# Performance work log

Measured on AMD Instinct MI355X. Metric: run time of the kernel, lower is better.

The kernel has to match this reference:

```python
import jax, jax.numpy as jnp
import numpy as np


def setup_inputs() -> dict:
    key = jax.random.key(0)
    ks = jax.random.split(key, 5)
    B, T, D = 1, 4096, 1024
    scale = 0.02
    return {
        "x": jax.random.normal(ks[0], (B, T, D), dtype=jnp.float32),
        "Wq": jax.random.normal(ks[1], (D, D), dtype=jnp.float32) * scale,
        "Wk": jax.random.normal(ks[2], (D, D), dtype=jnp.float32) * scale,
        "Wv": jax.random.normal(ks[3], (D, D), dtype=jnp.float32) * scale,
        "Wo": jax.random.normal(ks[4], (D, D), dtype=jnp.float32) * scale,
        "window": 128,
    }


def reference(x, Wq, Wk, Wv, Wo, window):
    # x: [B, T, D]; weights: [D, D] (torch nn.Linear layout: out = x @ W.T)
    B, T, D = x.shape
    H = 16
    dh = D // H

    def split_heads(y):
        # [B, T, D] -> [B, H, T, dh]
        return y.reshape(B, T, H, dh).transpose(0, 2, 1, 3)

    q = split_heads(x @ Wq.T)
    k = split_heads(x @ Wk.T)
    v = split_heads(x @ Wv.T)

    # causal sliding-window additive mask, [T, T]
    idx = jnp.arange(T)
    diff = idx[:, None] - idx[None, :]
    allowed = (diff >= 0) & (diff <= window)

    scale = 1.0 / jnp.sqrt(jnp.asarray(dh, dtype=q.dtype))
    scores = jnp.einsum('bhtd,bhsd->bhts', q, k) * scale  # [B,H,T,T]
    scores = jnp.where(allowed[None, None], scores, jnp.asarray(-jnp.inf, dtype=scores.dtype))
    attn = jax.nn.softmax(scores, axis=-1)
    out = jnp.einsum('bhts,bhsd->bhtd', attn, v)  # [B,H,T,dh]
    out = out.transpose(0, 2, 1, 3).reshape(B, T, D)
    return out @ Wo.T
```

## Files before the change

### kernel.cpp

```cpp
#include <hip/hip_runtime.h>
#include <hip/hip_bf16.h>

typedef __bf16 bf16_t;
typedef __bf16 bf16x8 __attribute__((ext_vector_type(8)));
typedef float f32x4 __attribute__((ext_vector_type(4)));

#define T_SEQ 4096
#define DM    1024
#define NH    16
#define DH    64

#define BM 128
#define BN 128
#define BK 64

typedef __attribute__((address_space(1))) void gvoid_t;
typedef __attribute__((address_space(3))) void lvoid_t;

__device__ __forceinline__ void gload_lds16(const void* g, void* l) {
    __builtin_amdgcn_global_load_lds((gvoid_t*)g, (lvoid_t*)l, 16, 0, 0);
}

__global__ __launch_bounds__(256) void cvt_all(
    const float* __restrict__ x,  const float* __restrict__ wq,
    const float* __restrict__ wk, const float* __restrict__ wv,
    const float* __restrict__ wo,
    bf16_t* __restrict__ xb, bf16_t* __restrict__ wqb, bf16_t* __restrict__ wkb,
    bf16_t* __restrict__ wvb, bf16_t* __restrict__ wob)
{
    const float* s; bf16_t* d; int n8;
    switch (blockIdx.y) {
        case 0:  s = x;  d = xb;  n8 = (T_SEQ * DM) / 8; break;
        case 1:  s = wq; d = wqb; n8 = (DM * DM) / 8;    break;
        case 2:  s = wk; d = wkb; n8 = (DM * DM) / 8;    break;
        case 3:  s = wv; d = wvb; n8 = (DM * DM) / 8;    break;
        default: s = wo; d = wob; n8 = (DM * DM) / 8;    break;
    }
    for (int i = blockIdx.x * 256 + threadIdx.x; i < n8; i += gridDim.x * 256) {
        float4 a = ((const float4*)s)[i * 2];
        float4 b = ((const float4*)s)[i * 2 + 1];
        bf16x8 o;
        o[0] = (bf16_t)a.x; o[1] = (bf16_t)a.y; o[2] = (bf16_t)a.z; o[3] = (bf16_t)a.w;
        o[4] = (bf16_t)b.x; o[5] = (bf16_t)b.y; o[6] = (bf16_t)b.z; o[7] = (bf16_t)b.w;
        ((bf16x8*)d)[i] = o;
    }
}

template<typename OT>
__global__ __launch_bounds__(256) void gemm_bt(
    const bf16_t* __restrict__ A,
    const bf16_t* __restrict__ B0, const bf16_t* __restrict__ B1, const bf16_t* __restrict__ B2,
    OT* __restrict__ C0, OT* __restrict__ C1, OT* __restrict__ C2,
    int M, int N, int K)
{
    const bf16_t* Bp; OT* Cp;
    if      (blockIdx.z == 0) { Bp = B0; Cp = C0; }
    else if (blockIdx.z == 1) { Bp = B1; Cp = C1; }
    else                      { Bp = B2; Cp = C2; }

    __shared__ __align__(16) bf16_t sA[BM * BK];
    __shared__ __align__(16) bf16_t sB[BN * BK];

    const int tid  = threadIdx.x;
    const int lane = tid & 63;
    const int w    = tid >> 6;
    const int wr   = w >> 1, wc = w & 1;
    const int l15  = lane & 15, lhi = lane >> 4;

    const int brow = blockIdx.x * BM;
    const int bcol = blockIdx.y * BN;

    f32x4 acc[4][4] = {};

    const int nkt = K / BK;
    for (int kt = 0; kt < nkt; ++kt) {
        __syncthreads();
        #pragma unroll
        for (int i = 0; i < 4; ++i) {
            int chunk = i * 256 + tid;
            int row   = chunk >> 3;
            int c8    = chunk & 7;
            int c8s   = c8 ^ (row & 7);
            const bf16_t* gA = A  + (size_t)(brow + row) * K + kt * BK + c8s * 8;
            const bf16_t* gB = Bp + (size_t)(bcol + row) * K + kt * BK + c8s * 8;
            gload_lds16(gA, &sA[chunk * 8]);
            gload_lds16(gB, &sB[chunk * 8]);
        }
        __syncthreads();

        #pragma unroll
        for (int kk = 0; kk < 2; ++kk) {
            bf16x8 af[4], bfr[4];
            #pragma unroll
            for (int m = 0; m < 4; ++m) {
                int r  = wr * 64 + m * 16 + l15;
                int c8 = (kk * 4 + lhi) ^ (r & 7);
                af[m] = *(const bf16x8*)(&sA[r * BK + c8 * 8]);
            }
            #pragma unroll
            for (int n = 0; n < 4; ++n) {
                int r  = wc * 64 + n * 16 + l15;
                int c8 = (kk * 4 + lhi) ^ (r & 7);
                bfr[n] = *(const bf16x8*)(&sB[r * BK + c8 * 8]);
            }
            #pragma unroll
            for (int m = 0; m < 4; ++m)
                #pragma unroll
                for (int n = 0; n < 4; ++n)
                    acc[m][n] = __builtin_amdgcn_mfma_f32_16x16x32_bf16(
                        af[m], bfr[n], acc[m][n], 0, 0, 0);
        }
    }

    #pragma unroll
    for (int m = 0; m < 4; ++m) {
        int rb = brow + wr * 64 + m * 16 + lhi * 4;
        #pragma unroll
        for (int n = 0; n < 4; ++n) {
            int cc = bcol + wc * 64 + n * 16 + l15;
            #pragma unroll
            for (int i = 0; i < 4; ++i)
                Cp[(size_t)(rb + i) * N + cc] = (OT)acc[m][n][i];
        }
    }
}

__global__ __launch_bounds__(256) void swa_attn(
    const bf16_t* __restrict__ Q, const bf16_t* __restrict__ K,
    const bf16_t* __restrict__ V, bf16_t* __restrict__ O,
    const int* __restrict__ winp)
{
    const int w    = winp[0];
    const int tid  = threadIdx.x;
    const int lane = tid & 63;
    const int wv   = tid >> 6;
    const int l15  = lane & 15, lhi = lane >> 4;
    const int h    = blockIdx.y;
    const int q0   = blockIdx.x * 64 + wv * 16;

    __shared__ __align__(16) bf16_t Pl[4][16 * 48];
    bf16_t* Pw = &Pl[wv][0];

    bf16x8 qf[2];
    #pragma unroll
    for (int c = 0; c < 2; ++c)
        qf[c] = *(const bf16x8*)(Q + (size_t)(q0 + l15) * DM + h * DH + c * 32 + lhi * 8);

    f32x4 acc[4] = {};
    f32x4 mrow = { -1e30f, -1e30f, -1e30f, -1e30f };
    f32x4 lrow = {};

    int ks = q0 - w; if (ks < 0) ks = 0; ks &= ~31;
    for (int kvs = ks; kvs <= q0 + 15; kvs += 32) {
        f32x4 s[2];
        #pragma unroll
        for (int hc = 0; hc < 2; ++hc) {
            f32x4 z = {};
            #pragma unroll
            for (int c = 0; c < 2; ++c) {
                bf16x8 kf = *(const bf16x8*)(K + (size_t)(kvs + hc * 16 + l15) * DM
                                               + h * DH + c * 32 + lhi * 8);
                z = __builtin_amdgcn_mfma_f32_16x16x32_bf16(qf[c], kf, z, 0, 0, 0);
            }
            #pragma unroll
            for (int i = 0; i < 4; ++i) {
                int qt = q0 + lhi * 4 + i;
                int kt = kvs + hc * 16 + l15;
                bool ok = (kt <= qt) && (qt - kt <= w);
                s[hc][i] = ok ? z[i] * 0.125f : -1e30f;
            }
        }
        f32x4 pm;
        #pragma unroll
        for (int i = 0; i < 4; ++i) pm[i] = fmaxf(s[0][i], s[1][i]);
        #pragma unroll
        for (int off = 1; off <= 8; off <<= 1)
            #pragma unroll
            for (int i = 0; i < 4; ++i)
                pm[i] = fmaxf(pm[i], __shfl_xor(pm[i], off));

        f32x4 mnew, alpha, p0, p1, rs;
        #pragma unroll
        for (int i = 0; i < 4; ++i) {
            mnew[i]  = fmaxf(mrow[i], pm[i]);
            alpha[i] = __expf(mrow[i] - mnew[i]);
            p0[i]    = __expf(s[0][i] - mnew[i]);
            p1[i]    = __expf(s[1][i] - mnew[i]);
            rs[i]    = p0[i] + p1[i];
        }
        #pragma unroll
        for (int off = 1; off <= 8; off <<= 1)
            #pragma unroll
            for (int i = 0; i < 4; ++i)
                rs[i] += __shfl_xor(rs[i], off);
        #pragma unroll
        for (int i = 0; i < 4; ++i) {
            lrow[i] = lrow[i] * alpha[i] + rs[i];
            mrow[i] = mnew[i];
        }
        #pragma unroll
        for (int nc = 0; nc < 4; ++nc)
            #pragma unroll
            for (int i = 0; i < 4; ++i) acc[nc][i] *= alpha[i];

        #pragma unroll
        for (int i = 0; i < 4; ++i) {
            int r = lhi * 4 + i;
            Pw[r * 48 + l15]      = (bf16_t)p0[i];
            Pw[r * 48 + 16 + l15] = (bf16_t)p1[i];
        }
        bf16x8 pa = *(const bf16x8*)(&Pw[l15 * 48 + lhi * 8]);

        #pragma unroll
        for (int nc = 0; nc < 4; ++nc) {
            bf16x8 vf;
            #pragma unroll
            for (int j = 0; j < 8; ++j)
                vf[j] = V[(size_t)(kvs + lhi * 8 + j) * DM + h * DH + nc * 16 + l15];
            acc[nc] = __builtin_amdgcn_mfma_f32_16x16x32_bf16(pa, vf, acc[nc], 0, 0, 0);
        }
    }

    #pragma unroll
    for (int nc = 0; nc < 4; ++nc)
        #pragma unroll
        for (int i = 0; i < 4; ++i) {
            float o = acc[nc][i] / lrow[i];
            O[(size_t)(q0 + lhi * 4 + i) * DM + h * DH + nc * 16 + l15] = (bf16_t)o;
        }
}

extern "C" void kernel_launch(void* const* d_in, const int* in_sizes, int n_in,
                              void* d_out, int out_size, void* d_ws, size_t ws_size,
                              hipStream_t stream)
{
    const float* x  = (const float*)d_in[0];
    const float* Wq = (const float*)d_in[1];
    const float* Wk = (const float*)d_in[2];
    const float* Wv = (const float*)d_in[3];
    const float* Wo = (const float*)d_in[4];
    const int*   wn = (const int*)d_in[5];
    float* out = (float*)d_out;

    bf16_t* ws = (bf16_t*)d_ws;
    const size_t nx = (size_t)T_SEQ * DM;
    const size_t nw = (size_t)DM * DM;
    bf16_t* xb  = ws;
    bf16_t* Wqb = xb + nx;
    bf16_t* Wkb = Wqb + nw;
    bf16_t* Wvb = Wkb + nw;
    bf16_t* Wob = Wvb + nw;
    bf16_t* Qb  = Wob + nw;
    bf16_t* Kb  = Qb + nx;
    bf16_t* Vb  = Kb + nx;
    bf16_t* Ab  = Vb + nx;

    dim3 g0(1024, 5, 1);
    cvt_all<<<g0, 256, 0, stream>>>(x, Wq, Wk, Wv, Wo, xb, Wqb, Wkb, Wvb, Wob);

    dim3 g1(T_SEQ / BM, DM / BN, 3);
    gemm_bt<bf16_t><<<g1, 256, 0, stream>>>(xb, Wqb, Wkb, Wvb, Qb, Kb, Vb, T_SEQ, DM, DM);

    dim3 g2(T_SEQ / 64, NH, 1);
    swa_attn<<<g2, 256, 0, stream>>>(Qb, Kb, Vb, Ab, wn);

    dim3 g3(T_SEQ / BM, DM / BN, 1);
    gemm_bt<float><<<g3, 256, 0, stream>>>(Ab, Wob, Wob, Wob, out, out, out, T_SEQ, DM, DM);
}
```

Before: 88.70 us.

## Process 32 query rows per wave and reuse K/V fragments across row groups

Each attention wave now handles two 16-row query groups over 64-key tiles. Every K and V fragment it loads feeds MFMAs for both groups, roughly halving global K/V traffic per query. The P staging buffer is enlarged and padded to hold the larger tile. The cost is higher register pressure, fewer blocks in the grid, and more masked work at the window edges. The conversion kernel's grid is also halved, which assumes it uses a grid-stride loop.

```diff
diff --git a/kernel.cpp b/kernel.cpp
--- a/kernel.cpp
+++ b/kernel.cpp
@@ -125,6 +125,7 @@
     }
 }
 
+#define PPAD 72
 __global__ __launch_bounds__(256) void swa_attn(
     const bf16_t* __restrict__ Q, const bf16_t* __restrict__ K,
     const bf16_t* __restrict__ V, bf16_t* __restrict__ O,
@@ -136,98 +137,139 @@
     const int wv   = tid >> 6;
     const int l15  = lane & 15, lhi = lane >> 4;
     const int h    = blockIdx.y;
-    const int q0   = blockIdx.x * 64 + wv * 16;
-
-    __shared__ __align__(16) bf16_t Pl[4][16 * 48];
+    const int q0   = blockIdx.x * 128 + wv * 32;
+
+    __shared__ __align__(16) bf16_t Pl[4][32 * PPAD];
     bf16_t* Pw = &Pl[wv][0];
 
-    bf16x8 qf[2];
+    const bf16_t* Qh = Q + (size_t)h * DH;
+    const bf16_t* Kh = K + (size_t)h * DH;
+    const bf16_t* Vh = V + (size_t)h * DH;
+
+    bf16x8 qf[2][2];
     #pragma unroll
-    for (int c = 0; c < 2; ++c)
-        qf[c] = *(const bf16x8*)(Q + (size_t)(q0 + l15) * DM + h * DH + c * 32 + lhi * 8);
-
-    f32x4 acc[4] = {};
-    f32x4 mrow = { -1e30f, -1e30f, -1e30f, -1e30f };
-    f32x4 lrow = {};
-
-    int ks = q0 - w; if (ks < 0) ks = 0; ks &= ~31;
-    for (int kvs = ks; kvs <= q0 + 15; kvs += 32) {
-        f32x4 s[2];
-        #pragma unroll
-        for (int hc = 0; hc < 2; ++hc) {
-            f32x4 z = {};
-            #pragma unroll
-            for (int c = 0; c < 2; ++c) {
-                bf16x8 kf = *(const bf16x8*)(K + (size_t)(kvs + hc * 16 + l15) * DM
-                                               + h * DH + c * 32 + lhi * 8);
-                z = __builtin_amdgcn_mfma_f32_16x16x32_bf16(qf[c], kf, z, 0, 0, 0);
-            }
+    for (int g = 0; g < 2; ++g)
+        #pragma unroll
+        for (int c = 0; c < 2; ++c)
+            qf[g][c] = *(const bf16x8*)(Qh + (size_t)(q0 + g * 16 + l15) * DM
+                                           + c * 32 + lhi * 8);
+
+    f32x4 acc[2][4] = {};
+    f32x4 mrow[2], lrow[2];
+    #pragma unroll
+    for (int g = 0; g < 2; ++g) {
+        mrow[g] = { -1e30f, -1e30f, -1e30f, -1e30f };
+        lrow[g] = {};
+    }
+
+    int ks = q0 - w; if (ks < 0) ks = 0; ks &= ~63;
+    for (int kvs = ks; kvs <= q0 + 31; kvs += 64) {
+        f32x4 s[2][4];
+        #pragma unroll
+        for (int hc = 0; hc < 4; ++hc) {
+            bf16x8 kf[2];
+            #pragma unroll
+            for (int c = 0; c < 2; ++c)
+                kf[c] = *(const bf16x8*)(Kh + (size_t)(kvs + hc * 16 + l15) * DM
+                                            + c * 32 + lhi * 8);
+            #pragma unroll
+            for (int g = 0; g < 2; ++g) {
+                f32x4 z = {};
+                z = __builtin_amdgcn_mfma_f32_16x16x32_bf16(qf[g][0], kf[0], z, 0, 0, 0);
+                z = __builtin_amdgcn_mfma_f32_16x16x32_bf16(qf[g][1], kf[1], z, 0, 0, 0);
+                #pragma unroll
+                for (int i = 0; i < 4; ++i) {
+                    int qt = q0 + g * 16 + lhi * 4 + i;
+                    int kt = kvs + hc * 16 + l15;
+                    bool ok = (kt <= qt) && (qt - kt <= w);
+                    s[g][hc][i] = ok ? z[i] * 0.125f : -1e30f;
+                }
+            }
+        }
+        #pragma unroll
+        for (int g = 0; g < 2; ++g) {
+            f32x4 pm;
+            #pragma unroll
+            for (int i = 0; i < 4; ++i)
+                pm[i] = fmaxf(fmaxf(s[g][0][i], s[g][1][i]),
+                              fmaxf(s[g][2][i], s[g][3][i]));
+            #pragma unroll
+            for (int off = 1; off <= 8; off <<= 1)
+                #pragma unroll
+                for (int i = 0; i < 4; ++i)
+                    pm[i] = fmaxf(pm[i], __shfl_xor(pm[i], off));
+
+            f32x4 mnew, alpha, rs;
             #pragma unroll
             for (int i = 0; i < 4; ++i) {
-                int qt = q0 + lhi * 4 + i;
-                int kt = kvs + hc * 16 + l15;
-                bool ok = (kt <= qt) && (qt - kt <= w);
-                s[hc][i] = ok ? z[i] * 0.125f : -1e30f;
-            }
-        }
-        f32x4 pm;
-        #pragma unroll
-        for (int i = 0; i < 4; ++i) pm[i] = fmaxf(s[0][i], s[1][i]);
-        #pragma unroll
-        for (int off = 1; off <= 8; off <<= 1)
-            #pragma unroll
-            for (int i = 0; i < 4; ++i)
-                pm[i] = fmaxf(pm[i], __shfl_xor(pm[i], off));
-
-        f32x4 mnew, alpha, p0, p1, rs;
-        #pragma unroll
-        for (int i = 0; i < 4; ++i) {
-            mnew[i]  = fmaxf(mrow[i], pm[i]);
-            alpha[i] = __expf(mrow[i] - mnew[i]);
-            p0[i]    = __expf(s[0][i] - mnew[i]);
-            p1[i]    = __expf(s[1][i] - mnew[i]);
-            rs[i]    = p0[i] + p1[i];
-        }
-        #pragma unroll
-        for (int off = 1; off <= 8; off <<= 1)
-            #pragma unroll
-            for (int i = 0; i < 4; ++i)
-                rs[i] += __shfl_xor(rs[i], off);
-        #pragma unroll
-        for (int i = 0; i < 4; ++i) {
-            lrow[i] = lrow[i] * alpha[i] + rs[i];
-            mrow[i] = mnew[i];
-        }
+                mnew[i]  = fmaxf(mrow[g][i], pm[i]);
+                alpha[i] = __expf(mrow[g][i] - mnew[i]);
+                rs[i]    = 0.f;
+            }
+            #pragma unroll
+            for (int hc = 0; hc < 4; ++hc)
+                #pragma unroll
+                for (int i = 0; i < 4; ++i) {
+                    float p = __expf(s[g][hc][i] - mnew[i]);
+                    s[g][hc][i] = p;
+                    rs[i] += p;
+                }
+            #pragma unroll
+            for (int off = 1; off <= 8; off <<= 1)
+                #pragma unroll
+                for (int i = 0; i < 4; ++i)
+                    rs[i] += __shfl_xor(rs[i], off);
+            #pragma unroll
+            for (int i = 0; i < 4; ++i) {
+                lrow[g][i] = lrow[g][i] * alpha[i] + rs[i];
+                mrow[g][i] = mnew[i];
+            }
+            #pragma unroll
+            for (int nc = 0; nc < 4; ++nc)
+                #pragma unroll
+                for (int i = 0; i < 4; ++i) acc[g][nc][i] *= alpha[i];
+
+            #pragma unroll
+            for (int hc = 0; hc < 4; ++hc)
+                #pragma unroll
+                for (int i = 0; i < 4; ++i)
+                    Pw[(g * 16 + lhi * 4 + i) * PPAD + hc * 16 + l15] =
+                        (bf16_t)s[g][hc][i];
+        }
+
+        bf16x8 pa[2][2];
+        #pragma unroll
+        for (int g = 0; g < 2; ++g)
+            #pragma unroll
+            for (int kk = 0; kk < 2; ++kk)
+                pa[g][kk] = *(const bf16x8*)(&Pw[(g * 16 + l15) * PPAD
+                                                + kk * 32 + lhi * 8]);
+        #pragma unroll
+        for (int kk = 0; kk < 2; ++kk)
+            #pragma unroll
+            for (int nc = 0; nc < 4; ++nc) {
+                bf16x8 vf;
+                #pragma unroll
+                for (int j = 0; j < 8; ++j)
+                    vf[j] = Vh[(size_t)(kvs + kk * 32 + lhi * 8 + j) * DM
+                               + nc * 16 + l15];
+                #pragma unroll
+                for (int g = 0; g < 2; ++g)
+                    acc[g][nc] = __builtin_amdgcn_mfma_f32_16x16x32_bf16(
+                        pa[g][kk], vf, acc[g][nc], 0, 0, 0);
+            }
+    }
+
+    #pragma unroll
+    for (int g = 0; g < 2; ++g)
         #pragma unroll
         for (int nc = 0; nc < 4; ++nc)
             #pragma unroll
-            for (int i = 0; i < 4; ++i) acc[nc][i] *= alpha[i];
-
-        #pragma unroll
-        for (int i = 0; i < 4; ++i) {
-            int r = lhi * 4 + i;
-            Pw[r * 48 + l15]      = (bf16_t)p0[i];
-            Pw[r * 48 + 16 + l15] = (bf16_t)p1[i];
-        }
-        bf16x8 pa = *(const bf16x8*)(&Pw[l15 * 48 + lhi * 8]);
-
-        #pragma unroll
-        for (int nc = 0; nc < 4; ++nc) {
-            bf16x8 vf;
-            #pragma unroll
-            for (int j = 0; j < 8; ++j)
-                vf[j] = V[(size_t)(kvs + lhi * 8 + j) * DM + h * DH + nc * 16 + l15];
-            acc[nc] = __builtin_amdgcn_mfma_f32_16x16x32_bf16(pa, vf, acc[nc], 0, 0, 0);
-        }
-    }
-
-    #pragma unroll
-    for (int nc = 0; nc < 4; ++nc)
-        #pragma unroll
-        for (int i = 0; i < 4; ++i) {
-            float o = acc[nc][i] / lrow[i];
-            O[(size_t)(q0 + lhi * 4 + i) * DM + h * DH + nc * 16 + l15] = (bf16_t)o;
-        }
+            for (int i = 0; i < 4; ++i) {
+                float o = acc[g][nc][i] / lrow[g][i];
+                O[(size_t)(q0 + g * 16 + lhi * 4 + i) * DM + h * DH
+                  + nc * 16 + l15] = (bf16_t)o;
+            }
 }
 
 extern "C" void kernel_launch(void* const* d_in, const int* in_sizes, int n_in,
@@ -255,13 +297,13 @@
     bf16_t* Vb  = Kb + nx;
     bf16_t* Ab  = Vb + nx;
 
-    dim3 g0(1024, 5, 1);
+    dim3 g0(512, 5, 1);
     cvt_all<<<g0, 256, 0, stream>>>(x, Wq, Wk, Wv, Wo, xb, Wqb, Wkb, Wvb, Wob);
 
     dim3 g1(T_SEQ / BM, DM / BN, 3);
     gemm_bt<bf16_t><<<g1, 256, 0, stream>>>(xb, Wqb, Wkb, Wvb, Qb, Kb, Vb, T_SEQ, DM, DM);
 
-    dim3 g2(T_SEQ / 64, NH, 1);
+    dim3 g2(T_SEQ / 128, NH, 1);
     swa_attn<<<g2, 256, 0, stream>>>(Qb, Kb, Vb, Ab, wn);
 
     dim3 g3(T_SEQ / BM, DM / BN, 1);
```

New measurement: 84.39 us. 4.9% less time.
